# Kernel tuning notes

Hardware: AMD Instinct MI355X
Metric: run time of the kernel (lower is better)

Reference implementation:

```python
import jax, jax.numpy as jnp
import numpy as np

# ---- architecture constants (from init_kwargs / arch_args) ----
B, CIN, H, W = 2, 128, 32, 32
COUT, K, PAD = 128, 3, 1
IB, FRAC, NSTREAMS = 8, 8, 8     # input bits, input frac bits, 1-bit streams
WB, NSLICES = 8, 8               # weight bits, 1-bit slices
ADC_BITS = 4
NSUB = 9                         # ceil(128*9 / subarray_size=128); 1152/9 = 128 (even chunks)


def ste_round(x):
    # straight-through round
    return x + jax.lax.stop_gradient(jnp.round(x) - x)


def unfold(x, k, pad):
    # torch F.unfold (im2col), channel-major (c, kh, kw) feature ordering
    xp = jnp.pad(x, ((0, 0), (0, 0), (pad, pad), (pad, pad)))
    Ho = x.shape[2] + 2 * pad - k + 1
    Wo = x.shape[3] + 2 * pad - k + 1
    cols = [xp[:, :, i:i + Ho, j:j + Wo] for i in range(k) for j in range(k)]
    p = jnp.stack(cols, axis=2)              # [B, C, k*k, Ho, Wo]
    return p.reshape(x.shape[0], -1, Ho * Wo), Ho, Wo


def bit_streams(patches):
    # quantize unsigned fixed-point then decompose into 1-bit streams (STE)
    xi = jnp.clip(ste_round(patches * (2.0 ** FRAC)), 0.0, 2.0 ** IB - 1.0)  # [B,F,P]
    shifts = 2.0 ** jnp.arange(NSTREAMS, dtype=jnp.float32)
    bits = jnp.floor(jax.lax.stop_gradient(xi)[..., None] / shifts) % 2.0
    share = xi[..., None] / (NSTREAMS * shifts)  # equal-split STE grad path (recombines to identity)
    return share + jax.lax.stop_gradient(bits - share)  # [B,F,P,S]


def bit_slices(w):
    # per-out-channel normalization, signed int quantization, pos/neg 1-bit slices (STE)
    norm = jax.lax.stop_gradient(jnp.max(jnp.abs(w.reshape(w.shape[0], -1)), axis=1))  # [O]
    Q = 2.0 ** WB - 1.0
    wi = ste_round(w / norm[:, None, None, None] * Q)  # in [-Q, Q]
    shifts = 2.0 ** jnp.arange(NSLICES, dtype=jnp.float32)

    def slices(m):
        b = jnp.floor(jax.lax.stop_gradient(m)[..., None] / shifts) % 2.0
        share = m[..., None] / (NSLICES * shifts)
        return share + jax.lax.stop_gradient(b - share)

    pos = slices(jax.nn.relu(wi)).reshape(w.shape[0], -1, NSLICES)   # [O, F, T]
    neg = slices(jax.nn.relu(-wi)).reshape(w.shape[0], -1, NSLICES)  # [O, F, T]
    return pos, neg, norm


def adc(ps):
    # N-bit ADC quantization of non-negative partial sums, dynamic full-scale, STE
    levels = 2.0 ** ADC_BITS - 1.0
    vmax = jnp.maximum(jax.lax.stop_gradient(jnp.max(ps)), 1e-6)
    step = vmax / levels
    return jnp.clip(ste_round(ps / step), 0.0, levels) * step


def _forward(inputs, weight):
    patches, Ho, Wo = unfold(inputs, K, PAD)          # [B, CIN*K*K, P]
    streams = bit_streams(patches)                     # [B, F, P, S]
    pos_w, neg_w, norm = bit_slices(weight)            # [O, F, T]
    ss = (2.0 ** jnp.arange(NSTREAMS, dtype=jnp.float32)).reshape(1, 1, 1, -1, 1)
    ts = (2.0 ** jnp.arange(NSLICES, dtype=jnp.float32)).reshape(1, 1, 1, 1, -1)

    s_chunks = jnp.split(streams, NSUB, axis=1)
    p_chunks = jnp.split(pos_w, NSUB, axis=1)
    n_chunks = jnp.split(neg_w, NSUB, axis=1)

    out = jnp.zeros((inputs.shape[0], COUT, Ho * Wo), jnp.float32)
    for sc, pc, nc in zip(s_chunks, p_chunks, n_chunks):  # fixed NSUB=9 subarrays
        pr = jnp.einsum('bfps,oft->bopst', sc, pc)  # [B,O,P,S,T] per-subarray MVM
        nr = jnp.einsum('bfps,oft->bopst', sc, nc)
        out = out + ((adc(pr) - adc(nr)) * ss * ts).sum(axis=(-2, -1))

    Q = 2.0 ** WB - 1.0
    out = out * norm[None, :, None] / Q / (2.0 ** IB)
    return out.reshape(inputs.shape[0], COUT, Ho, Wo)


def setup_inputs() -> dict:
    key = jax.random.key(0)
    k1, k2 = jax.random.split(key)
    inputs = jax.random.uniform(k1, (B, CIN, H, W), dtype=jnp.float32)
    fan_in = CIN * K * K
    weight = jax.random.normal(k2, (COUT, CIN, K, K), dtype=jnp.float32) * np.float32(np.sqrt(2.0 / fan_in))
    return {"inputs": inputs, "weight": weight}


def reference(inputs, weight):
    output = _forward(inputs, weight)
    adc_loss = jnp.float32(0.0)  # adc_custom_loss=False
    return output, adc_loss
```

## Files before the change

### kernel.cpp

```cpp
#include <hip/hip_runtime.h>
#include <stdint.h>

#define B_    2
#define CIN   128
#define HIMG  32
#define WIMG  32
#define COUT_ 128
#define PP    1024
#define FTOT  1152
#define NSUB  9
#define NS    8
#define NT    8

typedef int v4i __attribute__((ext_vector_type(4)));

#define OFF_NORM   0
#define OFF_MAXV   512
#define OFF_LUT    1024
#define OFF_WQP    4096
#define OFF_WQN    (4096 + 147456)
#define OFF_XQ     (4096 + 2*147456)

__global__ __launch_bounds__(256) void k_prep_w(const float* __restrict__ w,
                                                float* __restrict__ norm_out,
                                                uint8_t* __restrict__ wqp,
                                                uint8_t* __restrict__ wqn) {
    int o = blockIdx.x, tid = threadIdx.x;
    __shared__ float red[256];
    const float* wo = w + (size_t)o * FTOT;
    float m = 0.f;
    for (int f = tid; f < FTOT; f += 256) m = fmaxf(m, fabsf(wo[f]));
    red[tid] = m;
    __syncthreads();
    for (int s2 = 128; s2 > 0; s2 >>= 1) {
        if (tid < s2) red[tid] = fmaxf(red[tid], red[tid + s2]);
        __syncthreads();
    }
    float norm = red[0];
    if (tid == 0) norm_out[o] = norm;
    for (int f = tid; f < FTOT; f += 256) {
        double wi = rint(((double)wo[f] / (double)norm) * 255.0);
        wqp[(size_t)o * FTOT + f] = (uint8_t)(int)fmax(wi, 0.0);
        wqn[(size_t)o * FTOT + f] = (uint8_t)(int)fmax(-wi, 0.0);
    }
}

__global__ __launch_bounds__(256) void k_prep_x(const float* __restrict__ x,
                                                uint8_t* __restrict__ xq) {
    int gid = blockIdx.x * 256 + threadIdx.x;
    int fg = gid % 72;
    int rest = gid / 72;
    int p = rest & 1023;
    int b = rest >> 10;
    int py = p >> 5, px = p & 31;
    uint32_t dw[4] = {0, 0, 0, 0};
    #pragma unroll
    for (int j = 0; j < 16; ++j) {
        int f = fg * 16 + j;
        int c = f / 9, u = f % 9;
        int kh = u / 3, kw = u % 3;
        int y = py + kh - 1, xx = px + kw - 1;
        uint32_t xi = 0;
        if (y >= 0 && y < HIMG && xx >= 0 && xx < WIMG) {
            float v = x[(((size_t)b * CIN + c) * HIMG + y) * WIMG + xx];
            float q = rintf(v * 256.0f);
            q = fminf(fmaxf(q, 0.f), 255.f);
            xi = (uint32_t)q;
        }
        dw[j >> 2] |= xi << ((j & 3) * 8);
    }
    *reinterpret_cast<uint4*>(xq + (size_t)((b << 10) + p) * FTOT + fg * 16) =
        make_uint4(dw[0], dw[1], dw[2], dw[3]);
}

__device__ __forceinline__ v4i bitsel(uint4 d, int sh) {
    v4i r;
    r[0] = (int)((d.x >> sh) & 0x01010101u);
    r[1] = (int)((d.y >> sh) & 0x01010101u);
    r[2] = (int)((d.z >> sh) & 0x01010101u);
    r[3] = (int)((d.w >> sh) & 0x01010101u);
    return r;
}

__global__ __launch_bounds__(512) void k_max(const uint8_t* __restrict__ xq,
                                             const uint8_t* __restrict__ wqp,
                                             const uint8_t* __restrict__ wqn,
                                             uint32_t* __restrict__ maxv) {
    int tid = threadIdx.x, lane = tid & 63, wid = tid >> 6;
    int blk = blockIdx.x;
    int b = blk >> 9, r = blk & 511, ot = r >> 6, pt = r & 63;
    int s = wid;
    int col = lane & 15, kq = lane >> 4;
    int p = pt * 16 + col, oa = ot * 16 + col;
    __shared__ uint32_t smax[8][NSUB][2];

    const uint8_t* xbase = xq + (size_t)((b << 10) + p) * FTOT + kq * 16;
    const uint8_t* wpb = wqp + (size_t)oa * FTOT + kq * 16;
    const uint8_t* wnb = wqn + (size_t)oa * FTOT + kq * 16;

    for (int sub = 0; sub < NSUB; ++sub) {
        int fo = sub * 128;
        uint4 xg0 = *(const uint4*)(xbase + fo);
        uint4 xg1 = *(const uint4*)(xbase + fo + 64);
        v4i bf0 = bitsel(xg0, s), bf1 = bitsel(xg1, s);
        uint4 wp0 = *(const uint4*)(wpb + fo), wp1 = *(const uint4*)(wpb + fo + 64);
        uint4 wn0 = *(const uint4*)(wnb + fo), wn1 = *(const uint4*)(wnb + fo + 64);
        int mp = 0, mn = 0;
        #pragma unroll
        for (int t = 0; t < NT; ++t) {
            v4i acc = {0, 0, 0, 0};
            acc = __builtin_amdgcn_mfma_i32_16x16x64_i8(bitsel(wp0, t), bf0, acc, 0, 0, 0);
            acc = __builtin_amdgcn_mfma_i32_16x16x64_i8(bitsel(wp1, t), bf1, acc, 0, 0, 0);
            mp = max(max(acc[0], acc[1]), max(max(acc[2], acc[3]), mp));
            v4i acn = {0, 0, 0, 0};
            acn = __builtin_amdgcn_mfma_i32_16x16x64_i8(bitsel(wn0, t), bf0, acn, 0, 0, 0);
            acn = __builtin_amdgcn_mfma_i32_16x16x64_i8(bitsel(wn1, t), bf1, acn, 0, 0, 0);
            mn = max(max(acn[0], acn[1]), max(max(acn[2], acn[3]), mn));
        }
        #pragma unroll
        for (int off = 32; off > 0; off >>= 1) {
            mp = max(mp, __shfl_xor(mp, off));
            mn = max(mn, __shfl_xor(mn, off));
        }
        if (lane == 0) { smax[wid][sub][0] = (uint32_t)mp; smax[wid][sub][1] = (uint32_t)mn; }
    }
    __syncthreads();
    if (tid < 18) {
        int sub = tid >> 1, sg = tid & 1;
        uint32_t m = 0;
        #pragma unroll
        for (int w2 = 0; w2 < 8; ++w2) m = max(m, smax[w2][sub][sg]);
        atomicMax(&maxv[tid], m);
    }
}

__global__ void k_lut(const uint32_t* __restrict__ maxv, uint8_t* __restrict__ lut) {
    int i = threadIdx.x;
    for (int e = i; e < 18 * 129; e += 256) {
        int idx = e / 129, pr = e % 129;
        double vmaxd = fmax((double)maxv[idx], 1e-6);
        double step = vmaxd / 15.0;
        double q = rint((double)pr / step);
        q = fmin(fmax(q, 0.0), 15.0);
        lut[idx * 132 + pr] = (uint8_t)q;
    }
}

__global__ __launch_bounds__(512) void k_adc(const uint8_t* __restrict__ xq,
                                             const uint8_t* __restrict__ wqp,
                                             const uint8_t* __restrict__ wqn,
                                             const uint32_t* __restrict__ maxv,
                                             const uint8_t* __restrict__ lut,
                                             const float* __restrict__ norm,
                                             float* __restrict__ out) {
    int tid = threadIdx.x, lane = tid & 63, wid = tid >> 6;
    int blk = blockIdx.x;
    int b = blk >> 9, r = blk & 511, ot = r >> 6, pt = r & 63;
    int s = wid;
    int col = lane & 15, kq = lane >> 4;
    int p = pt * 16 + col, oa = ot * 16 + col;

    __shared__ uint8_t llut[4 * 2376];
    __shared__ int lred[8][64][4];
    {
        const uint32_t* l32 = (const uint32_t*)lut;
        uint32_t* s32 = (uint32_t*)llut;
        for (int i = tid; i < 594; i += 512) {
            uint32_t v = l32[i];
            #pragma unroll
            for (int c2 = 0; c2 < 4; ++c2) s32[c2 * 594 + i] = v;
        }
    }
    __syncthreads();
    const uint8_t* myl = llut + (lane & 3) * 2376;

    const uint8_t* xbase = xq + (size_t)((b << 10) + p) * FTOT + kq * 16;
    const uint8_t* wpb = wqp + (size_t)oa * FTOT + kq * 16;
    const uint8_t* wnb = wqn + (size_t)oa * FTOT + kq * 16;

    int run[4] = {0, 0, 0, 0};
    for (int sub = 0; sub < NSUB; ++sub) {
        int fo = sub * 128;
        uint4 xg0 = *(const uint4*)(xbase + fo);
        uint4 xg1 = *(const uint4*)(xbase + fo + 64);
        v4i bf0 = bitsel(xg0, s), bf1 = bitsel(xg1, s);
        uint4 wp0 = *(const uint4*)(wpb + fo), wp1 = *(const uint4*)(wpb + fo + 64);
        uint4 wn0 = *(const uint4*)(wnb + fo), wn1 = *(const uint4*)(wnb + fo + 64);
        const uint8_t* lp = myl + sub * 264;
        const uint8_t* ln = lp + 132;
        int vp = (int)maxv[sub * 2], vn = (int)maxv[sub * 2 + 1];
        uint32_t Sp[4] = {0, 0, 0, 0}, Sn[4] = {0, 0, 0, 0};
        #pragma unroll
        for (int t = 0; t < NT; ++t) {
            v4i acc = {0, 0, 0, 0};
            acc = __builtin_amdgcn_mfma_i32_16x16x64_i8(bitsel(wp0, t), bf0, acc, 0, 0, 0);
            acc = __builtin_amdgcn_mfma_i32_16x16x64_i8(bitsel(wp1, t), bf1, acc, 0, 0, 0);
            #pragma unroll
            for (int i = 0; i < 4; ++i) Sp[i] += (uint32_t)lp[acc[i]] << (s + t);
            v4i acn = {0, 0, 0, 0};
            acn = __builtin_amdgcn_mfma_i32_16x16x64_i8(bitsel(wn0, t), bf0, acn, 0, 0, 0);
            acn = __builtin_amdgcn_mfma_i32_16x16x64_i8(bitsel(wn1, t), bf1, acn, 0, 0, 0);
            #pragma unroll
            for (int i = 0; i < 4; ++i) Sn[i] += (uint32_t)ln[acn[i]] << (s + t);
        }
        #pragma unroll
        for (int i = 0; i < 4; ++i) run[i] += vp * (int)Sp[i] - vn * (int)Sn[i];
    }
    #pragma unroll
    for (int i = 0; i < 4; ++i) lred[wid][lane][i] = run[i];
    __syncthreads();
    if (tid < 256) {
        int lane2 = tid >> 2, i = tid & 3;
        long long s64 = 0;
        #pragma unroll
        for (int w2 = 0; w2 < 8; ++w2) s64 += (long long)lred[w2][lane2][i];
        int o = ot * 16 + (lane2 >> 4) * 4 + i;
        int pp2 = pt * 16 + (lane2 & 15);
        double v = (double)s64 * (double)norm[o] / 15.0 / 255.0 / 256.0;
        out[((size_t)(b * COUT_ + o)) * PP + pp2] = (float)v;
    }
    if (blk == 0 && tid == 0) out[(size_t)B_ * COUT_ * PP] = 0.0f;
}

extern "C" void kernel_launch(void* const* d_in, const int* in_sizes, int n_in,
                              void* d_out, int out_size, void* d_ws, size_t ws_size,
                              hipStream_t stream) {
    const float* x = (const float*)d_in[0];
    const float* w = (const float*)d_in[1];
    float* out = (float*)d_out;
    char* ws = (char*)d_ws;

    float* norm = (float*)(ws + OFF_NORM);
    uint32_t* maxv = (uint32_t*)(ws + OFF_MAXV);
    uint8_t* lut = (uint8_t*)(ws + OFF_LUT);
    uint8_t* wqp = (uint8_t*)(ws + OFF_WQP);
    uint8_t* wqn = (uint8_t*)(ws + OFF_WQN);
    uint8_t* xq  = (uint8_t*)(ws + OFF_XQ);

    hipMemsetAsync(maxv, 0, 18 * sizeof(uint32_t), stream);
    k_prep_w<<<128, 256, 0, stream>>>(w, norm, wqp, wqn);
    k_prep_x<<<576, 256, 0, stream>>>(x, xq);
    k_max<<<1024, 512, 0, stream>>>(xq, wqp, wqn, maxv);
    k_lut<<<1, 256, 0, stream>>>(maxv, lut);
    k_adc<<<1024, 512, 0, stream>>>(xq, wqp, wqn, maxv, lut, norm, out);
}
```

Before: 140.5 us.

## Replace ADC LUT lookups with verified arithmetic quantization and fold memset into prep

The k_lut kernel now searches for a float reciprocal and bias per subarray row such that rintf(pr*inv+bias) reproduces the double-precision LUT exactly for every reachable partial sum. k_adc then uses this FMA+rint path instead of shared-memory byte lookups, falling back to the global LUT only when no candidate matches. This drops the shared LUT replication and its syncthreads, and removes the memset launch by zeroing maxv inside k_prep_x. The cost is a brute-force search in a single-block kernel, plus a uniform branch per subarray in the hot loop.

Result: slower. 172.4 us (+22.7%).

```diff
diff --git a/kernel.cpp b/kernel.cpp
--- a/kernel.cpp
+++ b/kernel.cpp
@@ -11,11 +11,14 @@
 #define NSUB  9
 #define NS    8
 #define NT    8
+#define NROW  18
 
 typedef int v4i __attribute__((ext_vector_type(4)));
 
 #define OFF_NORM   0
 #define OFF_MAXV   512
+#define OFF_PRM    640
+#define OFF_PMODE  800
 #define OFF_LUT    1024
 #define OFF_WQP    4096
 #define OFF_WQN    (4096 + 147456)
@@ -46,7 +49,9 @@
 }
 
 __global__ __launch_bounds__(256) void k_prep_x(const float* __restrict__ x,
-                                                uint8_t* __restrict__ xq) {
+                                                uint8_t* __restrict__ xq,
+                                                uint32_t* __restrict__ maxv) {
+    if (blockIdx.x == 0 && threadIdx.x < NROW) maxv[threadIdx.x] = 0u;
     int gid = blockIdx.x * 256 + threadIdx.x;
     int fg = gid % 72;
     int rest = gid / 72;
@@ -125,7 +130,7 @@
         if (lane == 0) { smax[wid][sub][0] = (uint32_t)mp; smax[wid][sub][1] = (uint32_t)mn; }
     }
     __syncthreads();
-    if (tid < 18) {
+    if (tid < NROW) {
         int sub = tid >> 1, sg = tid & 1;
         uint32_t m = 0;
         #pragma unroll
@@ -134,15 +139,64 @@
     }
 }
 
-__global__ void k_lut(const uint32_t* __restrict__ maxv, uint8_t* __restrict__ lut) {
-    int i = threadIdx.x;
-    for (int e = i; e < 18 * 129; e += 256) {
+__device__ __forceinline__ float adc_arith(float fpr, float inv, float bias) {
+    return rintf(fmaf(fpr, inv, bias));
+}
+
+__global__ void k_lut(const uint32_t* __restrict__ maxv,
+                      uint8_t* __restrict__ lut,
+                      float* __restrict__ prm,
+                      int* __restrict__ pmode) {
+    __shared__ uint8_t codes[NROW][132];
+    __shared__ int best[NROW];
+    int tid = threadIdx.x;
+    if (tid < NROW) best[tid] = 0x7fffffff;
+    for (int e = tid; e < NROW * 129; e += 256) {
         int idx = e / 129, pr = e % 129;
         double vmaxd = fmax((double)maxv[idx], 1e-6);
         double step = vmaxd / 15.0;
         double q = rint((double)pr / step);
         q = fmin(fmax(q, 0.0), 15.0);
+        codes[idx][pr] = (uint8_t)q;
         lut[idx * 132 + pr] = (uint8_t)q;
+    }
+    __syncthreads();
+
+    const int NDI = 13, NBJ = 11, NC = NDI * NBJ;
+    const int di[NDI] = {0, -1, 1, -2, 2, -3, 3, -4, 4, -5, 5, -6, 6};
+    const float bl[NBJ] = {0.0f,
+                           -1.220703125e-4f, 1.220703125e-4f,
+                           -2.44140625e-4f,  2.44140625e-4f,
+                           -4.8828125e-4f,   4.8828125e-4f,
+                           -9.765625e-4f,    9.765625e-4f,
+                           -1.953125e-3f,    1.953125e-3f};
+    for (int task = tid; task < NROW * NC; task += 256) {
+        int row = task / NC, cand = task % NC;
+        int vmax = (int)maxv[row];
+        float inv0 = (float)(15.0 / fmax((double)vmax, 1e-6));
+        float inv = __int_as_float(__float_as_int(inv0) + di[cand % NDI]);
+        float bias = bl[cand / NDI];
+        bool ok = true;
+        for (int pr = 0; pr <= vmax; ++pr) {
+            if ((int)adc_arith((float)pr, inv, bias) != (int)codes[row][pr]) { ok = false; break; }
+        }
+        if (vmax == 0) ok = ((int)adc_arith(0.f, inv, bias) == 0);
+        if (ok) atomicMin(&best[row], cand);
+    }
+    __syncthreads();
+    if (tid < NROW) {
+        int cand = best[tid];
+        if (cand == 0x7fffffff) {
+            pmode[tid] = 1;
+            prm[tid * 2 + 0] = 0.f;
+            prm[tid * 2 + 1] = 0.f;
+        } else {
+            int vmax = (int)maxv[tid];
+            float inv0 = (float)(15.0 / fmax((double)vmax, 1e-6));
+            pmode[tid] = 0;
+            prm[tid * 2 + 0] = __int_as_float(__float_as_int(inv0) + di[cand % NDI]);
+            prm[tid * 2 + 1] = bl[cand / NDI];
+        }
     }
 }
 
@@ -151,6 +205,8 @@
                                              const uint8_t* __restrict__ wqn,
                                              const uint32_t* __restrict__ maxv,
                                              const uint8_t* __restrict__ lut,
+                                             const float* __restrict__ prm,
+                                             const int* __restrict__ pmode,
                                              const float* __restrict__ norm,
                                              float* __restrict__ out) {
     int tid = threadIdx.x, lane = tid & 63, wid = tid >> 6;
@@ -160,19 +216,7 @@
     int col = lane & 15, kq = lane >> 4;
     int p = pt * 16 + col, oa = ot * 16 + col;
 
-    __shared__ uint8_t llut[4 * 2376];
     __shared__ int lred[8][64][4];
-    {
-        const uint32_t* l32 = (const uint32_t*)lut;
-        uint32_t* s32 = (uint32_t*)llut;
-        for (int i = tid; i < 594; i += 512) {
-            uint32_t v = l32[i];
-            #pragma unroll
-            for (int c2 = 0; c2 < 4; ++c2) s32[c2 * 594 + i] = v;
-        }
-    }
-    __syncthreads();
-    const uint8_t* myl = llut + (lane & 3) * 2376;
 
     const uint8_t* xbase = xq + (size_t)((b << 10) + p) * FTOT + kq * 16;
     const uint8_t* wpb = wqp + (size_t)oa * FTOT + kq * 16;
@@ -186,25 +230,49 @@
         v4i bf0 = bitsel(xg0, s), bf1 = bitsel(xg1, s);
         uint4 wp0 = *(const uint4*)(wpb + fo), wp1 = *(const uint4*)(wpb + fo + 64);
         uint4 wn0 = *(const uint4*)(wnb + fo), wn1 = *(const uint4*)(wnb + fo + 64);
-        const uint8_t* lp = myl + sub * 264;
-        const uint8_t* ln = lp + 132;
-        int vp = (int)maxv[sub * 2], vn = (int)maxv[sub * 2 + 1];
-        uint32_t Sp[4] = {0, 0, 0, 0}, Sn[4] = {0, 0, 0, 0};
+
+        int rowp = sub * 2, rown = sub * 2 + 1;
+        float ivp = prm[rowp * 2], bvp = prm[rowp * 2 + 1];
+        float ivn = prm[rown * 2], bvn = prm[rown * 2 + 1];
+        int fbp = pmode[rowp], fbn = pmode[rown];
+        const uint8_t* glp = lut + rowp * 132;
+        const uint8_t* gln = lut + rown * 132;
+        int vp = (int)maxv[rowp], vn = (int)maxv[rown];
+
+        float Spf[4] = {0.f, 0.f, 0.f, 0.f}, Snf[4] = {0.f, 0.f, 0.f, 0.f};
         #pragma unroll
         for (int t = 0; t < NT; ++t) {
+            const float ct = (float)(1 << t);
             v4i acc = {0, 0, 0, 0};
             acc = __builtin_amdgcn_mfma_i32_16x16x64_i8(bitsel(wp0, t), bf0, acc, 0, 0, 0);
             acc = __builtin_amdgcn_mfma_i32_16x16x64_i8(bitsel(wp1, t), bf1, acc, 0, 0, 0);
-            #pragma unroll
-            for (int i = 0; i < 4; ++i) Sp[i] += (uint32_t)lp[acc[i]] << (s + t);
+            if (fbp == 0) {
+                #pragma unroll
+                for (int i = 0; i < 4; ++i)
+                    Spf[i] = fmaf(adc_arith((float)acc[i], ivp, bvp), ct, Spf[i]);
+            } else {
+                #pragma unroll
+                for (int i = 0; i < 4; ++i)
+                    Spf[i] = fmaf((float)glp[acc[i]], ct, Spf[i]);
+            }
             v4i acn = {0, 0, 0, 0};
             acn = __builtin_amdgcn_mfma_i32_16x16x64_i8(bitsel(wn0, t), bf0, acn, 0, 0, 0);
             acn = __builtin_amdgcn_mfma_i32_16x16x64_i8(bitsel(wn1, t), bf1, acn, 0, 0, 0);
-            #pragma unroll
-            for (int i = 0; i < 4; ++i) Sn[i] += (uint32_t)ln[acn[i]] << (s + t);
-        }
-        #pragma unroll
-        for (int i = 0; i < 4; ++i) run[i] += vp * (int)Sp[i] - vn * (int)Sn[i];
+            if (fbn == 0) {
+                #pragma unroll
+                for (int i = 0; i < 4; ++i)
+                    Snf[i] = fmaf(adc_arith((float)acn[i], ivn, bvn), ct, Snf[i]);
+            } else {
+                #pragma unroll
+                for (int i = 0; i < 4; ++i)
+                    Snf[i] = fmaf((float)gln[acn[i]], ct, Snf[i]);
+            }
+        }
+        #pragma unroll
+        for (int i = 0; i < 4; ++i) {
+            int Sp = (int)Spf[i], Sn = (int)Snf[i];
+            run[i] += vp * (Sp << s) - vn * (Sn << s);
+        }
     }
     #pragma unroll
     for (int i = 0; i < 4; ++i) lred[wid][lane][i] = run[i];
@@ -232,15 +300,16 @@
 
     float* norm = (float*)(ws + OFF_NORM);
     uint32_t* maxv = (uint32_t*)(ws + OFF_MAXV);
+    float* prm = (float*)(ws + OFF_PRM);
+    int* pmode = (int*)(ws + OFF_PMODE);
     uint8_t* lut = (uint8_t*)(ws + OFF_LUT);
     uint8_t* wqp = (uint8_t*)(ws + OFF_WQP);
     uint8_t* wqn = (uint8_t*)(ws + OFF_WQN);
     uint8_t* xq  = (uint8_t*)(ws + OFF_XQ);
 
-    hipMemsetAsync(maxv, 0, 18 * sizeof(uint32_t), stream);
     k_prep_w<<<128, 256, 0, stream>>>(w, norm, wqp, wqn);
-    k_prep_x<<<576, 256, 0, stream>>>(x, xq);
+    k_prep_x<<<576, 256, 0, stream>>>(x, xq, maxv);
     k_max<<<1024, 512, 0, stream>>>(xq, wqp, wqn, maxv);
-    k_lut<<<1, 256, 0, stream>>>(maxv, lut);
-    k_adc<<<1024, 512, 0, stream>>>(xq, wqp, wqn, maxv, lut, norm, out);
-}
+    k_lut<<<1, 256, 0, stream>>>(maxv, lut, prm, pmode);
+    k_adc<<<1024, 512, 0, stream>>>(xq, wqp, wqn, maxv, lut, prm, pmode, norm, out);
+}
```

## Replace ADC LUT lookups with exact multiply-shift and remap waves to weight slices

Applied to the files above, without the earlier changes.

The k_lut kernel now searches, per subarray row, for a fixed-point multiplier and offset that reproduce the ADC quantization table exactly. k_adc then computes codes with a mul24, add and shift instead of LDS table lookups, falling back to the global LUT when no exact multiplier exists. Both MFMA kernels move to 256-thread blocks where each wave handles two weight slices across all eight input bit streams, so weight bit extraction is hoisted and the input bit patterns are kept in registers, at the cost of higher register pressure. The memset is folded into k_prep_x to drop a separate launch.

New measurement: 146.1 us. 3.9% more time.

```diff
diff --git a/kernel.cpp b/kernel.cpp
--- a/kernel.cpp
+++ b/kernel.cpp
@@ -11,11 +11,14 @@
 #define NSUB  9
 #define NS    8
 #define NT    8
+#define NROW  18
 
 typedef int v4i __attribute__((ext_vector_type(4)));
 
 #define OFF_NORM   0
 #define OFF_MAXV   512
+#define OFF_MB     640
+#define OFF_PMODE  800
 #define OFF_LUT    1024
 #define OFF_WQP    4096
 #define OFF_WQN    (4096 + 147456)
@@ -46,7 +49,9 @@
 }
 
 __global__ __launch_bounds__(256) void k_prep_x(const float* __restrict__ x,
-                                                uint8_t* __restrict__ xq) {
+                                                uint8_t* __restrict__ xq,
+                                                uint32_t* __restrict__ maxv) {
+    if (blockIdx.x == 0 && threadIdx.x < NROW) maxv[threadIdx.x] = 0u;
     int gid = blockIdx.x * 256 + threadIdx.x;
     int fg = gid % 72;
     int rest = gid / 72;
@@ -82,17 +87,16 @@
     return r;
 }
 
-__global__ __launch_bounds__(512) void k_max(const uint8_t* __restrict__ xq,
-                                             const uint8_t* __restrict__ wqp,
-                                             const uint8_t* __restrict__ wqn,
-                                             uint32_t* __restrict__ maxv) {
+__global__ __launch_bounds__(256, 3) void k_max(const uint8_t* __restrict__ xq,
+                                                const uint8_t* __restrict__ wqp,
+                                                const uint8_t* __restrict__ wqn,
+                                                uint32_t* __restrict__ maxv) {
     int tid = threadIdx.x, lane = tid & 63, wid = tid >> 6;
     int blk = blockIdx.x;
-    int b = blk >> 9, r = blk & 511, ot = r >> 6, pt = r & 63;
-    int s = wid;
+    int b = blk >> 9, ot = (blk >> 6) & 7, pt = blk & 63;
     int col = lane & 15, kq = lane >> 4;
     int p = pt * 16 + col, oa = ot * 16 + col;
-    __shared__ uint32_t smax[8][NSUB][2];
+    __shared__ uint32_t smax[4][NSUB][2];
 
     const uint8_t* xbase = xq + (size_t)((b << 10) + p) * FTOT + kq * 16;
     const uint8_t* wpb = wqp + (size_t)oa * FTOT + kq * 16;
@@ -102,20 +106,29 @@
         int fo = sub * 128;
         uint4 xg0 = *(const uint4*)(xbase + fo);
         uint4 xg1 = *(const uint4*)(xbase + fo + 64);
-        v4i bf0 = bitsel(xg0, s), bf1 = bitsel(xg1, s);
+        v4i bf[NS][2];
+        #pragma unroll
+        for (int s = 0; s < NS; ++s) { bf[s][0] = bitsel(xg0, s); bf[s][1] = bitsel(xg1, s); }
         uint4 wp0 = *(const uint4*)(wpb + fo), wp1 = *(const uint4*)(wpb + fo + 64);
         uint4 wn0 = *(const uint4*)(wnb + fo), wn1 = *(const uint4*)(wnb + fo + 64);
+
         int mp = 0, mn = 0;
         #pragma unroll
-        for (int t = 0; t < NT; ++t) {
-            v4i acc = {0, 0, 0, 0};
-            acc = __builtin_amdgcn_mfma_i32_16x16x64_i8(bitsel(wp0, t), bf0, acc, 0, 0, 0);
-            acc = __builtin_amdgcn_mfma_i32_16x16x64_i8(bitsel(wp1, t), bf1, acc, 0, 0, 0);
-            mp = max(max(acc[0], acc[1]), max(max(acc[2], acc[3]), mp));
-            v4i acn = {0, 0, 0, 0};
-            acn = __builtin_amdgcn_mfma_i32_16x16x64_i8(bitsel(wn0, t), bf0, acn, 0, 0, 0);
-            acn = __builtin_amdgcn_mfma_i32_16x16x64_i8(bitsel(wn1, t), bf1, acn, 0, 0, 0);
-            mn = max(max(acn[0], acn[1]), max(max(acn[2], acn[3]), mn));
+        for (int tt = 0; tt < 2; ++tt) {
+            int t = wid * 2 + tt;
+            v4i ap0 = bitsel(wp0, t), ap1 = bitsel(wp1, t);
+            v4i an0 = bitsel(wn0, t), an1 = bitsel(wn1, t);
+            #pragma unroll
+            for (int s = 0; s < NS; ++s) {
+                v4i acc = {0, 0, 0, 0};
+                acc = __builtin_amdgcn_mfma_i32_16x16x64_i8(ap0, bf[s][0], acc, 0, 0, 0);
+                acc = __builtin_amdgcn_mfma_i32_16x16x64_i8(ap1, bf[s][1], acc, 0, 0, 0);
+                mp = max(mp, max(max(acc[0], acc[1]), max(acc[2], acc[3])));
+                v4i acn = {0, 0, 0, 0};
+                acn = __builtin_amdgcn_mfma_i32_16x16x64_i8(an0, bf[s][0], acn, 0, 0, 0);
+                acn = __builtin_amdgcn_mfma_i32_16x16x64_i8(an1, bf[s][1], acn, 0, 0, 0);
+                mn = max(mn, max(max(acn[0], acn[1]), max(acn[2], acn[3])));
+            }
         }
         #pragma unroll
         for (int off = 32; off > 0; off >>= 1) {
@@ -125,54 +138,78 @@
         if (lane == 0) { smax[wid][sub][0] = (uint32_t)mp; smax[wid][sub][1] = (uint32_t)mn; }
     }
     __syncthreads();
-    if (tid < 18) {
+    if (tid < NROW) {
         int sub = tid >> 1, sg = tid & 1;
-        uint32_t m = 0;
-        #pragma unroll
-        for (int w2 = 0; w2 < 8; ++w2) m = max(m, smax[w2][sub][sg]);
+        uint32_t m = max(max(smax[0][sub][sg], smax[1][sub][sg]),
+                         max(smax[2][sub][sg], smax[3][sub][sg]));
         atomicMax(&maxv[tid], m);
     }
 }
 
-__global__ void k_lut(const uint32_t* __restrict__ maxv, uint8_t* __restrict__ lut) {
-    int i = threadIdx.x;
-    for (int e = i; e < 18 * 129; e += 256) {
-        int idx = e / 129, pr = e % 129;
-        double vmaxd = fmax((double)maxv[idx], 1e-6);
+__global__ __launch_bounds__(256) void k_lut(const uint32_t* __restrict__ maxv,
+                                             uint8_t* __restrict__ lut,
+                                             uint2* __restrict__ mb,
+                                             int* __restrict__ pmode) {
+    int row = blockIdx.x, tid = threadIdx.x;
+    __shared__ uint8_t codes[132];
+    __shared__ int bestm;
+    if (tid == 0) bestm = 0x7fffffff;
+    int vmax = (int)maxv[row];
+    for (int pr = tid; pr < 129; pr += 256) {
+        double vmaxd = fmax((double)vmax, 1e-6);
         double step = vmaxd / 15.0;
         double q = rint((double)pr / step);
         q = fmin(fmax(q, 0.0), 15.0);
-        lut[idx * 132 + pr] = (uint8_t)q;
-    }
-}
-
-__global__ __launch_bounds__(512) void k_adc(const uint8_t* __restrict__ xq,
-                                             const uint8_t* __restrict__ wqp,
-                                             const uint8_t* __restrict__ wqn,
-                                             const uint32_t* __restrict__ maxv,
-                                             const uint8_t* __restrict__ lut,
-                                             const float* __restrict__ norm,
-                                             float* __restrict__ out) {
+        codes[pr] = (uint8_t)q;
+        lut[row * 132 + pr] = (uint8_t)q;
+    }
+    __syncthreads();
+    int ve = max(vmax, 1);
+    int m0 = (983040 + ve / 2) / ve;
+    int m = m0 - 128 + tid;
+    if (m >= 1) {
+        int L = 0, U = 0x7fffffff;
+        for (int pr = 0; pr <= vmax && pr <= 128; ++pr) {
+            int c = codes[pr];
+            int lo = (c << 16) - pr * m;
+            int hi = ((c + 1) << 16) - 1 - pr * m;
+            L = max(L, lo);
+            U = min(U, hi);
+            if (L > U) break;
+        }
+        if (L <= U) atomicMin(&bestm, m);
+    }
+    __syncthreads();
+    if (tid == 0) {
+        if (bestm == 0x7fffffff) {
+            pmode[row] = 1;
+            mb[row] = make_uint2(0u, 0u);
+        } else {
+            int L = 0;
+            for (int pr = 0; pr <= vmax && pr <= 128; ++pr)
+                L = max(L, ((int)codes[pr] << 16) - pr * bestm);
+            pmode[row] = 0;
+            mb[row] = make_uint2((uint32_t)bestm, (uint32_t)L);
+        }
+    }
+}
+
+__global__ __launch_bounds__(256, 3) void k_adc(const uint8_t* __restrict__ xq,
+                                                const uint8_t* __restrict__ wqp,
+                                                const uint8_t* __restrict__ wqn,
+                                                const uint32_t* __restrict__ maxv,
+                                                const uint8_t* __restrict__ lut,
+                                                const uint2* __restrict__ mb,
+                                                const int* __restrict__ pmode,
+                                                const float* __restrict__ norm,
+                                                float* __restrict__ out) {
     int tid = threadIdx.x, lane = tid & 63, wid = tid >> 6;
     int blk = blockIdx.x;
-    int b = blk >> 9, r = blk & 511, ot = r >> 6, pt = r & 63;
-    int s = wid;
+    int b = blk >> 9, ot = (blk >> 6) & 7, pt = blk & 63;
     int col = lane & 15, kq = lane >> 4;
     int p = pt * 16 + col, oa = ot * 16 + col;
 
-    __shared__ uint8_t llut[4 * 2376];
-    __shared__ int lred[8][64][4];
-    {
-        const uint32_t* l32 = (const uint32_t*)lut;
-        uint32_t* s32 = (uint32_t*)llut;
-        for (int i = tid; i < 594; i += 512) {
-            uint32_t v = l32[i];
-            #pragma unroll
-            for (int c2 = 0; c2 < 4; ++c2) s32[c2 * 594 + i] = v;
-        }
-    }
-    __syncthreads();
-    const uint8_t* myl = llut + (lane & 3) * 2376;
+    __shared__ int lred[4][64][4];
 
     const uint8_t* xbase = xq + (size_t)((b << 10) + p) * FTOT + kq * 16;
     const uint8_t* wpb = wqp + (size_t)oa * FTOT + kq * 16;
@@ -183,37 +220,64 @@
         int fo = sub * 128;
         uint4 xg0 = *(const uint4*)(xbase + fo);
         uint4 xg1 = *(const uint4*)(xbase + fo + 64);
-        v4i bf0 = bitsel(xg0, s), bf1 = bitsel(xg1, s);
+        v4i bf[NS][2];
+        #pragma unroll
+        for (int s = 0; s < NS; ++s) { bf[s][0] = bitsel(xg0, s); bf[s][1] = bitsel(xg1, s); }
         uint4 wp0 = *(const uint4*)(wpb + fo), wp1 = *(const uint4*)(wpb + fo + 64);
         uint4 wn0 = *(const uint4*)(wnb + fo), wn1 = *(const uint4*)(wnb + fo + 64);
-        const uint8_t* lp = myl + sub * 264;
-        const uint8_t* ln = lp + 132;
-        int vp = (int)maxv[sub * 2], vn = (int)maxv[sub * 2 + 1];
+
+        int rowp = sub * 2, rown = sub * 2 + 1;
+        uint2 mbp = mb[rowp], mbn = mb[rown];
+        int fbp = pmode[rowp], fbn = pmode[rown];
+        const uint8_t* glp = lut + rowp * 132;
+        const uint8_t* gln = lut + rown * 132;
+        int vp = (int)maxv[rowp], vn = (int)maxv[rown];
+
         uint32_t Sp[4] = {0, 0, 0, 0}, Sn[4] = {0, 0, 0, 0};
         #pragma unroll
-        for (int t = 0; t < NT; ++t) {
-            v4i acc = {0, 0, 0, 0};
-            acc = __builtin_amdgcn_mfma_i32_16x16x64_i8(bitsel(wp0, t), bf0, acc, 0, 0, 0);
-            acc = __builtin_amdgcn_mfma_i32_16x16x64_i8(bitsel(wp1, t), bf1, acc, 0, 0, 0);
+        for (int tt = 0; tt < 2; ++tt) {
+            int t = wid * 2 + tt;
+            v4i ap0 = bitsel(wp0, t), ap1 = bitsel(wp1, t);
+            v4i an0 = bitsel(wn0, t), an1 = bitsel(wn1, t);
             #pragma unroll
-            for (int i = 0; i < 4; ++i) Sp[i] += (uint32_t)lp[acc[i]] << (s + t);
-            v4i acn = {0, 0, 0, 0};
-            acn = __builtin_amdgcn_mfma_i32_16x16x64_i8(bitsel(wn0, t), bf0, acn, 0, 0, 0);
-            acn = __builtin_amdgcn_mfma_i32_16x16x64_i8(bitsel(wn1, t), bf1, acn, 0, 0, 0);
-            #pragma unroll
-            for (int i = 0; i < 4; ++i) Sn[i] += (uint32_t)ln[acn[i]] << (s + t);
-        }
-        #pragma unroll
-        for (int i = 0; i < 4; ++i) run[i] += vp * (int)Sp[i] - vn * (int)Sn[i];
+            for (int s = 0; s < NS; ++s) {
+                int st = s + t;
+                v4i acc = {0, 0, 0, 0};
+                acc = __builtin_amdgcn_mfma_i32_16x16x64_i8(ap0, bf[s][0], acc, 0, 0, 0);
+                acc = __builtin_amdgcn_mfma_i32_16x16x64_i8(ap1, bf[s][1], acc, 0, 0, 0);
+                if (fbp == 0) {
+                    #pragma unroll
+                    for (int i = 0; i < 4; ++i)
+                        Sp[i] += (((__umul24((uint32_t)acc[i], mbp.x) + mbp.y) >> 16) & 15u) << st;
+                } else {
+                    #pragma unroll
+                    for (int i = 0; i < 4; ++i) Sp[i] += (uint32_t)glp[acc[i]] << st;
+                }
+                v4i acn = {0, 0, 0, 0};
+                acn = __builtin_amdgcn_mfma_i32_16x16x64_i8(an0, bf[s][0], acn, 0, 0, 0);
+                acn = __builtin_amdgcn_mfma_i32_16x16x64_i8(an1, bf[s][1], acn, 0, 0, 0);
+                if (fbn == 0) {
+                    #pragma unroll
+                    for (int i = 0; i < 4; ++i)
+                        Sn[i] += (((__umul24((uint32_t)acn[i], mbn.x) + mbn.y) >> 16) & 15u) << st;
+                } else {
+                    #pragma unroll
+                    for (int i = 0; i < 4; ++i) Sn[i] += (uint32_t)gln[acn[i]] << st;
+                }
+            }
+        }
+        #pragma unroll
+        for (int i = 0; i < 4; ++i)
+            run[i] += (int)__umul24((uint32_t)vp, Sp[i]) - (int)__umul24((uint32_t)vn, Sn[i]);
     }
     #pragma unroll
     for (int i = 0; i < 4; ++i) lred[wid][lane][i] = run[i];
     __syncthreads();
-    if (tid < 256) {
+    {
         int lane2 = tid >> 2, i = tid & 3;
         long long s64 = 0;
         #pragma unroll
-        for (int w2 = 0; w2 < 8; ++w2) s64 += (long long)lred[w2][lane2][i];
+        for (int w2 = 0; w2 < 4; ++w2) s64 += (long long)lred[w2][lane2][i];
         int o = ot * 16 + (lane2 >> 4) * 4 + i;
         int pp2 = pt * 16 + (lane2 & 15);
         double v = (double)s64 * (double)norm[o] / 15.0 / 255.0 / 256.0;
@@ -232,15 +296,16 @@
 
     float* norm = (float*)(ws + OFF_NORM);
     uint32_t* maxv = (uint32_t*)(ws + OFF_MAXV);
+    uint2* mb = (uint2*)(ws + OFF_MB);
+    int* pmode = (int*)(ws + OFF_PMODE);
     uint8_t* lut = (uint8_t*)(ws + OFF_LUT);
     uint8_t* wqp = (uint8_t*)(ws + OFF_WQP);
     uint8_t* wqn = (uint8_t*)(ws + OFF_WQN);
     uint8_t* xq  = (uint8_t*)(ws + OFF_XQ);
 
-    hipMemsetAsync(maxv, 0, 18 * sizeof(uint32_t), stream);
     k_prep_w<<<128, 256, 0, stream>>>(w, norm, wqp, wqn);
-    k_prep_x<<<576, 256, 0, stream>>>(x, xq);
-    k_max<<<1024, 512, 0, stream>>>(xq, wqp, wqn, maxv);
-    k_lut<<<1, 256, 0, stream>>>(maxv, lut);
-    k_adc<<<1024, 512, 0, stream>>>(xq, wqp, wqn, maxv, lut, norm, out);
-}
+    k_prep_x<<<576, 256, 0, stream>>>(x, xq, maxv);
+    k_max<<<1024, 256, 0, stream>>>(xq, wqp, wqn, maxv);
+    k_lut<<<NROW, 256, 0, stream>>>(maxv, lut, mb, pmode);
+    k_adc<<<1024, 256, 0, stream>>>(xq, wqp, wqn, maxv, lut, mb, pmode, norm, out);
+}
```
